# Kernel tuning notes

Hardware: AMD Instinct MI355X
Metric: run time of the kernel (lower is better)

The kernel has to match this reference:

```python
import jax, jax.numpy as jnp
import numpy as np

LN_EPS = 1e-5


def _layer_norm(x, g, b):
    mu = jnp.mean(x, axis=-1, keepdims=True)
    var = jnp.mean(jnp.square(x - mu), axis=-1, keepdims=True)
    return (x - mu) * jax.lax.rsqrt(var + LN_EPS) * g + b


def setup_inputs() -> dict:
    key = jax.random.key(0)
    ks = jax.random.split(key, 8)
    B, S, D = 1, 4096, 1024
    scale = 1.0 / np.sqrt(D)  # keep activations sane (kaiming-ish)
    return {
        "sequences": jax.random.normal(ks[0], (B, S, D), dtype=jnp.float32),
        "W_q": jax.random.normal(ks[1], (D, D), dtype=jnp.float32) * scale,
        "W_k": jax.random.normal(ks[2], (D, D), dtype=jnp.float32) * scale,
        "W_v": jax.random.normal(ks[3], (D, D), dtype=jnp.float32) * scale,
        "W_o": jax.random.normal(ks[4], (D, D), dtype=jnp.float32) * scale,
        "out_w": jax.random.normal(ks[5], (D, D), dtype=jnp.float32) * scale,
        "out_b": jnp.zeros((D,), dtype=jnp.float32),
        "ln_attn_g": jnp.ones((D,), dtype=jnp.float32),
        "ln_attn_b": jnp.zeros((D,), dtype=jnp.float32),
        "ln_lin_g": jnp.ones((D,), dtype=jnp.float32),
        "ln_lin_b": jnp.zeros((D,), dtype=jnp.float32),
    }


def reference(sequences, W_q, W_k, W_v, W_o, out_w, out_b,
              ln_attn_g, ln_attn_b, ln_lin_g, ln_lin_b):
    B, S, D = sequences.shape
    H = 16
    Hd = D // H
    # input_dim == embedding_dim -> no input projection (input_layer is None)
    x = sequences
    q = jnp.einsum('bsd,de->bse', x, W_q)
    k = jnp.einsum('bsd,de->bse', x, W_k)
    v = jnp.einsum('bsd,de->bse', x, W_v)

    def heads(t):  # [B,S,D] -> [B,H,S,Hd]
        return t.reshape(B, S, H, Hd).transpose(0, 2, 1, 3)

    q, k, v = heads(q), heads(k), heads(v)
    scores = jnp.einsum('bhqd,bhkd->bhqk', q, k) / np.sqrt(Hd)  # [B,H,S,S]
    probs = jax.nn.softmax(scores, axis=-1)
    ctx = jnp.einsum('bhqk,bhkd->bhqd', probs, v)
    attn = ctx.transpose(0, 2, 1, 3).reshape(B, S, D)
    mha = _layer_norm(x + jnp.einsum('bsd,de->bse', attn, W_o),
                      ln_attn_g, ln_attn_b)
    lin = jnp.einsum('bsd,ed->bse', mha, out_w) + out_b  # torch Linear: x @ W.T + b
    out = jax.nn.relu(_layer_norm(lin + mha, ln_lin_g, ln_lin_b))
    return out
```

## Files before the change

kernel.cpp:

```cpp
#include <hip/hip_runtime.h>
#include <cstdint>
#include <math.h>

typedef __attribute__((ext_vector_type(8))) short bf16x8;
typedef __attribute__((ext_vector_type(4))) float f32x4;
typedef __attribute__((ext_vector_type(4))) unsigned short u16x4;

__device__ __forceinline__ unsigned short f2bf(float f) {
  union { float f; unsigned int u; } c; c.f = f;
  unsigned int u = c.u;
  return (unsigned short)((u + 0x7FFFu + ((u >> 16) & 1u)) >> 16);
}
__device__ __forceinline__ float bf2f(unsigned short u) {
  return __uint_as_float(((unsigned int)u) << 16);
}

__device__ __forceinline__ unsigned int pack_trunc(float a, float b) {
  return __builtin_amdgcn_perm(__float_as_uint(b), __float_as_uint(a), 0x07060302u);
}

__device__ __forceinline__ float fmax3(float a, float b, float c) {
  return fmaxf(fmaxf(a, b), c);
}

__device__ __forceinline__ void gload_lds16(const void* g, void* l) {
  __builtin_amdgcn_global_load_lds(
      (const __attribute__((address_space(1))) unsigned int*)g,
      (__attribute__((address_space(3))) unsigned int*)l, 16, 0, 0);
}

#define FSYNC(N) do {                                        \
    asm volatile("s_waitcnt vmcnt(" N ")" ::: "memory");     \
    __builtin_amdgcn_s_barrier();                            \
    __builtin_amdgcn_sched_barrier(0);                       \
  } while (0)

__global__ __launch_bounds__(256)
void k_prep(const float* __restrict__ x, unsigned short* __restrict__ xb,
            const float* __restrict__ out_w, unsigned short* __restrict__ OwB,
            const float* __restrict__ w0, const float* __restrict__ w1,
            const float* __restrict__ w2, const float* __restrict__ w3,
            unsigned short* __restrict__ o012, unsigned short* __restrict__ o3) {
  __shared__ float t[32][33];
  const int b = blockIdx.x;
  if (b < 4096) {
    const int m = b >> 10, rem = b & 1023;
    const float* in = m == 0 ? w0 : m == 1 ? w1 : m == 2 ? w2 : w3;
    unsigned short* out = m < 3 ? o012 + (size_t)m * 1048576 : o3;
    const int r0 = (rem >> 5) << 5, c0 = (rem & 31) << 5;
    const int tx = threadIdx.x & 31, ty = threadIdx.x >> 5;
#pragma unroll
    for (int rr = ty; rr < 32; rr += 8) t[rr][tx] = in[(size_t)(r0 + rr) * 1024 + c0 + tx];
    __syncthreads();
#pragma unroll
    for (int cc = ty; cc < 32; cc += 8)
      out[(size_t)(c0 + cc) * 1024 + r0 + tx] = f2bf(t[tx][cc]);
  } else {
    int i = (b - 4096) * 256 + threadIdx.x;
    const float* in;
    unsigned short* out;
    if (i < 1048576) { in = x; out = xb; }
    else { i -= 1048576; if (i >= 262144) return; in = out_w; out = OwB; }
    float4 v = ((const float4*)in)[i];
    u16x4 o;
    o.x = f2bf(v.x); o.y = f2bf(v.y); o.z = f2bf(v.z); o.w = f2bf(v.w);
    ((u16x4*)out)[i] = o;
  }
}

template <int MODE>
__global__ __launch_bounds__(256)
void k_gemm_bt(const unsigned short* __restrict__ A, const unsigned short* __restrict__ BT,
               void* __restrict__ C, unsigned short* __restrict__ VT,
               int M, int N, int K) {
  const int VCOL0 = 2048;
  __shared__ __align__(16) unsigned short As[2][128 * 32];
  __shared__ __align__(16) unsigned short Bs[2][128 * 32];
  const int tid = threadIdx.x;
  const int wid = tid >> 6, lane = tid & 63;
  const int l16 = lane & 15, krow = lane >> 4;
  const int m0 = blockIdx.x * 128, n0 = blockIdx.y * 128;
  const int wr = wid >> 1, wc = wid & 1;

  f32x4 acc[4][4] = {};

  auto stageG = [&](int buf, int k0) {
#pragma unroll
    for (int j = 0; j < 2; j++) {
      int f = j * 256 + tid;
      gload_lds16(A  + (size_t)(m0 + (f >> 2)) * K + k0 + (f & 3) * 8,
                  (char*)As[buf] + (size_t)(j * 256 + wid * 64) * 16);
      gload_lds16(BT + (size_t)(n0 + (f >> 2)) * K + k0 + (f & 3) * 8,
                  (char*)Bs[buf] + (size_t)(j * 256 + wid * 64) * 16);
    }
  };
  auto comp = [&](int buf) {
    bf16x8 a[4], b[4];
#pragma unroll
    for (int i = 0; i < 4; i++) {
      a[i] = *(const bf16x8*)&As[buf][(wr * 64 + i * 16 + l16) * 32 + krow * 8];
      b[i] = *(const bf16x8*)&Bs[buf][(wc * 64 + i * 16 + l16) * 32 + krow * 8];
    }
#pragma unroll
    for (int mi = 0; mi < 4; mi++)
#pragma unroll
      for (int ni = 0; ni < 4; ni++)
        acc[mi][ni] = __builtin_amdgcn_mfma_f32_16x16x32_bf16(a[mi], b[ni], acc[mi][ni], 0, 0, 0);
  };

  stageG(0, 0);
  __syncthreads();
  for (int k0 = 0; k0 < K; k0 += 64) {
    if (k0 + 32 < K) stageG(1, k0 + 32);
    comp(0);
    __syncthreads();
    if (k0 + 64 < K) stageG(0, k0 + 64);
    comp(1);
    __syncthreads();
  }

  if (MODE == 2 && n0 >= VCOL0) {
#pragma unroll
    for (int mi = 0; mi < 4; mi++)
#pragma unroll
      for (int ni = 0; ni < 4; ni++) {
        int col = n0 - VCOL0 + wc * 64 + ni * 16 + l16;
        int row = m0 + wr * 64 + mi * 16 + krow * 4;
        int u0 = row & 63;
        int rowp = (row & ~63) | (u0 & 32) | ((u0 & 12) << 1) | (((u0 >> 4) & 1) << 2);
        uint2 w;
        w.x = (unsigned)f2bf(acc[mi][ni][0]) | ((unsigned)f2bf(acc[mi][ni][1]) << 16);
        w.y = (unsigned)f2bf(acc[mi][ni][2]) | ((unsigned)f2bf(acc[mi][ni][3]) << 16);
        *(uint2*)&VT[(size_t)col * 4096 + rowp] = w;
      }
    return;
  }

#pragma unroll
  for (int mi = 0; mi < 4; mi++)
#pragma unroll
    for (int ni = 0; ni < 4; ni++)
#pragma unroll
      for (int r = 0; r < 4; r++) {
        int row = m0 + wr * 64 + mi * 16 + krow * 4 + r;
        int col = n0 + wc * 64 + ni * 16 + l16;
        float v = acc[mi][ni][r];
        if (MODE) ((unsigned short*)C)[(size_t)row * N + col] = f2bf(v);
        else      ((float*)C)[(size_t)row * N + col] = v;
      }
}

template <int OUTBF>
__global__ __launch_bounds__(256)
void k_gemm_bt_n64(const unsigned short* __restrict__ A, const unsigned short* __restrict__ BT,
                   void* __restrict__ C, int M, int N, int K) {
  __shared__ __align__(16) unsigned short As[2][128 * 32];
  __shared__ __align__(16) unsigned short Bs[2][64 * 32];
  const int tid = threadIdx.x;
  const int wid = tid >> 6, lane = tid & 63;
  const int l16 = lane & 15, krow = lane >> 4;
  const int m0 = blockIdx.x * 128, n0 = blockIdx.y * 64;
  const int wr = wid >> 1, wc = wid & 1;

  f32x4 acc[4][2] = {};

  auto stageG = [&](int buf, int k0) {
#pragma unroll
    for (int j = 0; j < 2; j++) {
      int f = j * 256 + tid;
      gload_lds16(A + (size_t)(m0 + (f >> 2)) * K + k0 + (f & 3) * 8,
                  (char*)As[buf] + (size_t)(j * 256 + wid * 64) * 16);
    }
    gload_lds16(BT + (size_t)(n0 + (tid >> 2)) * K + k0 + (tid & 3) * 8,
                (char*)Bs[buf] + (size_t)(wid * 64) * 16);
  };
  auto comp = [&](int buf) {
    bf16x8 a[4], b[2];
#pragma unroll
    for (int i = 0; i < 4; i++)
      a[i] = *(const bf16x8*)&As[buf][(wr * 64 + i * 16 + l16) * 32 + krow * 8];
#pragma unroll
    for (int i = 0; i < 2; i++)
      b[i] = *(const bf16x8*)&Bs[buf][(wc * 32 + i * 16 + l16) * 32 + krow * 8];
#pragma unroll
    for (int mi = 0; mi < 4; mi++)
#pragma unroll
      for (int ni = 0; ni < 2; ni++)
        acc[mi][ni] = __builtin_amdgcn_mfma_f32_16x16x32_bf16(a[mi], b[ni], acc[mi][ni], 0, 0, 0);
  };

  stageG(0, 0);
  __syncthreads();
  for (int k0 = 0; k0 < K; k0 += 64) {
    if (k0 + 32 < K) stageG(1, k0 + 32);
    comp(0);
    __syncthreads();
    if (k0 + 64 < K) stageG(0, k0 + 64);
    comp(1);
    __syncthreads();
  }

#pragma unroll
  for (int mi = 0; mi < 4; mi++)
#pragma unroll
    for (int ni = 0; ni < 2; ni++)
#pragma unroll
      for (int r = 0; r < 4; r++) {
        int row = m0 + wr * 64 + mi * 16 + krow * 4 + r;
        int col = n0 + wc * 32 + ni * 16 + l16;
        float v = acc[mi][ni][r];
        if (OUTBF) ((unsigned short*)C)[(size_t)row * N + col] = f2bf(v);
        else       ((float*)C)[(size_t)row * N + col] = v;
      }
}

__global__ __launch_bounds__(512)
void k_flash(const unsigned short* __restrict__ QKV, const unsigned short* __restrict__ Vt,
             unsigned short* __restrict__ ctx) {
  __shared__ __align__(16) unsigned short LDS[32768];
  const int tid = threadIdx.x, wid = tid >> 6, lane = tid & 63;
  const int l16 = lane & 15, krow = lane >> 4;
  const int bid = blockIdx.x;
  const int swz = (bid & 7) * 64 + (bid >> 3);
  const int head = swz >> 5, qb = swz & 31;
  const float SC = 0.125f * 1.44269504089f;

  bf16x8 qf[2];
#pragma unroll
  for (int ks = 0; ks < 2; ks++) {
    int row = qb * 128 + wid * 16 + l16;
    qf[ks] = *(const bf16x8*)&QKV[(size_t)row * 3072 + head * 64 + ks * 32 + krow * 8];
  }

  unsigned koff[2][4];
#pragma unroll
  for (int ks = 0; ks < 2; ks++)
#pragma unroll
    for (int ni = 0; ni < 4; ni++) {
      int row = ni * 16 + l16;
      koff[ks][ni] = row * 128 + (((ks * 4 + krow) ^ (row & 7)) << 4);
    }

  const unsigned short* kSrc;
  const unsigned short* vSrc;
  {
    int row = tid >> 3, sch = (tid & 7) ^ (row & 7);
    kSrc = QKV + (size_t)row * 3072 + 1024 + head * 64 + sch * 8;
    vSrc = Vt + (size_t)(head * 64 + row) * 4096 + sch * 8;
  }
  char* dK = (char*)LDS + wid * 1024;
  char* dV = (char*)LDS + 8192 + wid * 1024;

  f32x4 oaccT[4] = {};
  float mrun = -INFINITY;
  float lrun = 0.f;

  auto stage = [&](const int B) {
    gload_lds16(kSrc, dK + B);
    gload_lds16(vSrc, dV + B);
    kSrc += 64 * 3072;
    vSrc += 64;
  };

  auto body = [&](const int B) {
    const char* L = (const char*)LDS;

    f32x4 sacc[4] = {};
    __builtin_amdgcn_s_setprio(1);
#pragma unroll
    for (int ks = 0; ks < 2; ks++)
#pragma unroll
      for (int ni = 0; ni < 4; ni++) {
        bf16x8 kf = *(const bf16x8*)(L + B + koff[ks][ni]);
        sacc[ni] = __builtin_amdgcn_mfma_f32_16x16x32_bf16(kf, qf[ks], sacc[ni], 0, 0, 0);
      }
    __builtin_amdgcn_s_setprio(0);

    float a = fmax3(sacc[0][0], sacc[0][1], sacc[0][2]);
    a = fmax3(a, sacc[0][3], sacc[1][0]);
    a = fmax3(a, sacc[1][1], sacc[1][2]);
    a = fmax3(a, sacc[1][3], sacc[2][0]);
    a = fmax3(a, sacc[2][1], sacc[2][2]);
    a = fmax3(a, sacc[2][3], sacc[3][0]);
    a = fmax3(a, sacc[3][1], sacc[3][2]);
    a = fmaxf(a, sacc[3][3]);

    if (__ballot(__builtin_fmaf(a, SC, -mrun) > 8.f)) {
      a = fmaxf(a, __shfl_xor(a, 16));
      a = fmaxf(a, __shfl_xor(a, 32));
      float mnew = fmaxf(mrun, a * SC);
      float al = __builtin_amdgcn_exp2f(mrun - mnew);
      lrun *= al;
      mrun = mnew;
#pragma unroll
      for (int di = 0; di < 4; di++)
#pragma unroll
        for (int r = 0; r < 4; r++) oaccT[di][r] *= al;
    }

    float ps[4];
#pragma unroll
    for (int ni = 0; ni < 4; ni++) {
      float p0 = __builtin_amdgcn_exp2f(__builtin_fmaf(sacc[ni][0], SC, -mrun));
      float p1 = __builtin_amdgcn_exp2f(__builtin_fmaf(sacc[ni][1], SC, -mrun));
      float p2 = __builtin_amdgcn_exp2f(__builtin_fmaf(sacc[ni][2], SC, -mrun));
      float p3 = __builtin_amdgcn_exp2f(__builtin_fmaf(sacc[ni][3], SC, -mrun));
      sacc[ni][0] = p0; sacc[ni][1] = p1; sacc[ni][2] = p2; sacc[ni][3] = p3;
      ps[ni] = (p0 + p1) + (p2 + p3);
    }
    lrun += (ps[0] + ps[1]) + (ps[2] + ps[3]);

    union PB { unsigned int w[4]; bf16x8 v; };
    PB pb[2];
#pragma unroll
    for (int ks = 0; ks < 2; ks++) {
      pb[ks].w[0] = pack_trunc(sacc[2 * ks][0],     sacc[2 * ks][1]);
      pb[ks].w[1] = pack_trunc(sacc[2 * ks][2],     sacc[2 * ks][3]);
      pb[ks].w[2] = pack_trunc(sacc[2 * ks + 1][0], sacc[2 * ks + 1][1]);
      pb[ks].w[3] = pack_trunc(sacc[2 * ks + 1][2], sacc[2 * ks + 1][3]);
    }

    __builtin_amdgcn_s_setprio(1);
#pragma unroll
    for (int ks = 0; ks < 2; ks++)
#pragma unroll
      for (int di = 0; di < 4; di++) {
        bf16x8 av = *(const bf16x8*)(L + B + 8192 + koff[ks][di]);
        oaccT[di] = __builtin_amdgcn_mfma_f32_16x16x32_bf16(av, pb[ks].v, oaccT[di], 0, 0, 0);
      }
    __builtin_amdgcn_s_setprio(0);
  };

  stage(0);
  stage(16384);
  stage(32768);

  for (int t = 0; t < 60; t += 4) {
    FSYNC("4"); stage(49152); body(0);
    FSYNC("4"); stage(0);     body(16384);
    FSYNC("4"); stage(16384); body(32768);
    FSYNC("4"); stage(32768); body(49152);
  }
  FSYNC("4"); stage(49152); body(0);
  FSYNC("4"); body(16384);
  FSYNC("2"); body(32768);
  FSYNC("0"); body(49152);

  float lr = lrun;
  lr += __shfl_xor(lr, 16);
  lr += __shfl_xor(lr, 32);
  float li = 1.0f / lr;
  int row = qb * 128 + wid * 16 + l16;
#pragma unroll
  for (int di = 0; di < 4; di++) {
    uint2 w;
    w.x = (unsigned)f2bf(oaccT[di][0] * li) | ((unsigned)f2bf(oaccT[di][1] * li) << 16);
    w.y = (unsigned)f2bf(oaccT[di][2] * li) | ((unsigned)f2bf(oaccT[di][3] * li) << 16);
    *(uint2*)&ctx[(size_t)row * 1024 + head * 64 + di * 16 + krow * 4] = w;
  }
}

__global__ __launch_bounds__(256)
void k_ln_res(const float* __restrict__ base, const unsigned short* __restrict__ add,
              const float* __restrict__ g, const float* __restrict__ bb,
              unsigned short* __restrict__ outb) {
  const int r = blockIdx.x, tid = threadIdx.x;
  float4 v = ((const float4*)(base + (size_t)r * 1024))[tid];
  {
    u16x4 w = ((const u16x4*)(add + (size_t)r * 1024))[tid];
    v.x += bf2f(w.x); v.y += bf2f(w.y); v.z += bf2f(w.z); v.w += bf2f(w.w);
  }
  float s1 = v.x + v.y + v.z + v.w;
  float s2 = v.x * v.x + v.y * v.y + v.z * v.z + v.w * v.w;
#pragma unroll
  for (int off = 32; off >= 1; off >>= 1) { s1 += __shfl_xor(s1, off); s2 += __shfl_xor(s2, off); }
  __shared__ float red[8];
  if ((tid & 63) == 0) { red[tid >> 6] = s1; red[4 + (tid >> 6)] = s2; }
  __syncthreads();
  s1 = red[0] + red[1] + red[2] + red[3];
  s2 = red[4] + red[5] + red[6] + red[7];
  const float mu = s1 * (1.0f / 1024.0f);
  const float var = s2 * (1.0f / 1024.0f) - mu * mu;
  const float rs = rsqrtf(var + 1e-5f);
  float4 gv = ((const float4*)g)[tid];
  float4 bv = ((const float4*)bb)[tid];
  u16x4 o;
  o.x = f2bf((v.x - mu) * rs * gv.x + bv.x);
  o.y = f2bf((v.y - mu) * rs * gv.y + bv.y);
  o.z = f2bf((v.z - mu) * rs * gv.z + bv.z);
  o.w = f2bf((v.w - mu) * rs * gv.w + bv.w);
  ((u16x4*)(outb + (size_t)r * 1024))[tid] = o;
}

__global__ __launch_bounds__(256)
void k_ln2(const unsigned short* __restrict__ lin, const unsigned short* __restrict__ mha,
           const float* __restrict__ ob, const float* __restrict__ g,
           const float* __restrict__ bb, float* __restrict__ out) {
  const int r = blockIdx.x, tid = threadIdx.x;
  float4 v;
  {
    u16x4 a = ((const u16x4*)(lin + (size_t)r * 1024))[tid];
    u16x4 w = ((const u16x4*)(mha + (size_t)r * 1024))[tid];
    float4 o = ((const float4*)ob)[tid];
    v.x = bf2f(a.x) + bf2f(w.x) + o.x;
    v.y = bf2f(a.y) + bf2f(w.y) + o.y;
    v.z = bf2f(a.z) + bf2f(w.z) + o.z;
    v.w = bf2f(a.w) + bf2f(w.w) + o.w;
  }
  float s1 = v.x + v.y + v.z + v.w;
  float s2 = v.x * v.x + v.y * v.y + v.z * v.z + v.w * v.w;
#pragma unroll
  for (int off = 32; off >= 1; off >>= 1) { s1 += __shfl_xor(s1, off); s2 += __shfl_xor(s2, off); }
  __shared__ float red[8];
  if ((tid & 63) == 0) { red[tid >> 6] = s1; red[4 + (tid >> 6)] = s2; }
  __syncthreads();
  s1 = red[0] + red[1] + red[2] + red[3];
  s2 = red[4] + red[5] + red[6] + red[7];
  const float mu = s1 * (1.0f / 1024.0f);
  const float var = s2 * (1.0f / 1024.0f) - mu * mu;
  const float rs = rsqrtf(var + 1e-5f);
  float4 gv = ((const float4*)g)[tid];
  float4 bv = ((const float4*)bb)[tid];
  float4 y;
  y.x = fmaxf(0.f, (v.x - mu) * rs * gv.x + bv.x);
  y.y = fmaxf(0.f, (v.y - mu) * rs * gv.y + bv.y);
  y.z = fmaxf(0.f, (v.z - mu) * rs * gv.z + bv.z);
  y.w = fmaxf(0.f, (v.w - mu) * rs * gv.w + bv.w);
  ((float4*)(out + (size_t)r * 1024))[tid] = y;
}

extern "C" void kernel_launch(void* const* d_in, const int* in_sizes, int n_in,
                              void* d_out, int out_size, void* d_ws, size_t ws_size,
                              hipStream_t stream) {
  (void)in_sizes; (void)n_in; (void)out_size; (void)ws_size;
  const float* x     = (const float*)d_in[0];
  const float* Wq    = (const float*)d_in[1];
  const float* Wk    = (const float*)d_in[2];
  const float* Wv    = (const float*)d_in[3];
  const float* Wo    = (const float*)d_in[4];
  const float* out_w = (const float*)d_in[5];
  const float* out_b = (const float*)d_in[6];
  const float* g1    = (const float*)d_in[7];
  const float* b1    = (const float*)d_in[8];
  const float* g2    = (const float*)d_in[9];
  const float* b2    = (const float*)d_in[10];
  float* out = (float*)d_out;

  const size_t MB = 1ull << 20;
  char* ws = (char*)d_ws;
  unsigned short* xb    = (unsigned short*)(ws + 0);
  unsigned short* WqkvT = (unsigned short*)(ws + 8 * MB);
  unsigned short* OwB   = (unsigned short*)(ws + 16 * MB);
  unsigned short* QKV   = (unsigned short*)(ws + 18 * MB);
  unsigned short* Vt    = (unsigned short*)(ws + 42 * MB);
  unsigned short* ctx   = (unsigned short*)(ws + 50 * MB);
  unsigned short* WoT   = (unsigned short*)(ws + 58 * MB);
  unsigned short* proj  = (unsigned short*)(ws + 0);
  unsigned short* mhaB  = (unsigned short*)(ws + 34 * MB);
  unsigned short* lin   = (unsigned short*)(ws + 42 * MB);

  k_prep<<<9216, 256, 0, stream>>>(x, xb, out_w, OwB, Wq, Wk, Wv, Wo, WqkvT, WoT);

  k_gemm_bt<2><<<dim3(32, 24), 256, 0, stream>>>(xb, WqkvT, QKV, Vt, 4096, 3072, 1024);
  k_flash<<<512, 512, 0, stream>>>(QKV, Vt, ctx);
  k_gemm_bt_n64<1><<<dim3(32, 16), 256, 0, stream>>>(ctx, WoT, proj, 4096, 1024, 1024);
  k_ln_res<<<4096, 256, 0, stream>>>(x, proj, g1, b1, mhaB);
  k_gemm_bt_n64<1><<<dim3(32, 16), 256, 0, stream>>>(mhaB, OwB, lin, 4096, 1024, 1024);
  k_ln2<<<4096, 256, 0, stream>>>(lin, mhaB, out_b, g2, b2, out);
}
```

Baseline: 179.7 us.

## Process two query tiles per wave in flash attention with 256-thread blocks

The flash-attention kernel now uses 4 waves per block instead of 8. Each wave handles 32 query rows (two 16-row MFMA tiles), so every K/V fragment read from LDS feeds two MFMAs. To keep the same 64-key tile per stage, each thread issues twice as many global-to-LDS loads, and the vmcnt waits double to match. This halves LDS reads per MFMA and shared per-block overhead, but doubles accumulator and score registers per wave and halves the number of waves available to hide latency.

```diff
diff --git a/kernel.cpp b/kernel.cpp
--- a/kernel.cpp
+++ b/kernel.cpp
@@ -214,7 +214,7 @@
       }
 }
 
-__global__ __launch_bounds__(512)
+__global__ __launch_bounds__(256)
 void k_flash(const unsigned short* __restrict__ QKV, const unsigned short* __restrict__ Vt,
              unsigned short* __restrict__ ctx) {
   __shared__ __align__(16) unsigned short LDS[32768];
@@ -225,12 +225,14 @@
   const int head = swz >> 5, qb = swz & 31;
   const float SC = 0.125f * 1.44269504089f;
 
-  bf16x8 qf[2];
-#pragma unroll
-  for (int ks = 0; ks < 2; ks++) {
-    int row = qb * 128 + wid * 16 + l16;
-    qf[ks] = *(const bf16x8*)&QKV[(size_t)row * 3072 + head * 64 + ks * 32 + krow * 8];
-  }
+  bf16x8 qf[2][2];
+#pragma unroll
+  for (int mi = 0; mi < 2; mi++)
+#pragma unroll
+    for (int ks = 0; ks < 2; ks++) {
+      int row = qb * 128 + wid * 32 + mi * 16 + l16;
+      qf[mi][ks] = *(const bf16x8*)&QKV[(size_t)row * 3072 + head * 64 + ks * 32 + krow * 8];
+    }
 
   unsigned koff[2][4];
 #pragma unroll
@@ -251,13 +253,15 @@
   char* dK = (char*)LDS + wid * 1024;
   char* dV = (char*)LDS + 8192 + wid * 1024;
 
-  f32x4 oaccT[4] = {};
-  float mrun = -INFINITY;
-  float lrun = 0.f;
+  f32x4 oaccT[2][4] = {};
+  float mrun[2] = {-INFINITY, -INFINITY};
+  float lrun[2] = {0.f, 0.f};
 
   auto stage = [&](const int B) {
-    gload_lds16(kSrc, dK + B);
-    gload_lds16(vSrc, dV + B);
+    gload_lds16(kSrc,             dK + B);
+    gload_lds16(kSrc + 32 * 3072, dK + B + 4096);
+    gload_lds16(vSrc,             dV + B);
+    gload_lds16(vSrc + 32 * 4096, dV + B + 4096);
     kSrc += 64 * 3072;
     vSrc += 64;
   };
@@ -265,60 +269,76 @@
   auto body = [&](const int B) {
     const char* L = (const char*)LDS;
 
-    f32x4 sacc[4] = {};
+    f32x4 sacc[2][4] = {};
     __builtin_amdgcn_s_setprio(1);
 #pragma unroll
     for (int ks = 0; ks < 2; ks++)
 #pragma unroll
       for (int ni = 0; ni < 4; ni++) {
         bf16x8 kf = *(const bf16x8*)(L + B + koff[ks][ni]);
-        sacc[ni] = __builtin_amdgcn_mfma_f32_16x16x32_bf16(kf, qf[ks], sacc[ni], 0, 0, 0);
+#pragma unroll
+        for (int mi = 0; mi < 2; mi++)
+          sacc[mi][ni] = __builtin_amdgcn_mfma_f32_16x16x32_bf16(kf, qf[mi][ks], sacc[mi][ni], 0, 0, 0);
       }
     __builtin_amdgcn_s_setprio(0);
 
-    float a = fmax3(sacc[0][0], sacc[0][1], sacc[0][2]);
-    a = fmax3(a, sacc[0][3], sacc[1][0]);
-    a = fmax3(a, sacc[1][1], sacc[1][2]);
-    a = fmax3(a, sacc[1][3], sacc[2][0]);
-    a = fmax3(a, sacc[2][1], sacc[2][2]);
-    a = fmax3(a, sacc[2][3], sacc[3][0]);
-    a = fmax3(a, sacc[3][1], sacc[3][2]);
-    a = fmaxf(a, sacc[3][3]);
-
-    if (__ballot(__builtin_fmaf(a, SC, -mrun) > 8.f)) {
-      a = fmaxf(a, __shfl_xor(a, 16));
-      a = fmaxf(a, __shfl_xor(a, 32));
-      float mnew = fmaxf(mrun, a * SC);
-      float al = __builtin_amdgcn_exp2f(mrun - mnew);
-      lrun *= al;
-      mrun = mnew;
-#pragma unroll
-      for (int di = 0; di < 4; di++)
-#pragma unroll
-        for (int r = 0; r < 4; r++) oaccT[di][r] *= al;
-    }
-
-    float ps[4];
-#pragma unroll
-    for (int ni = 0; ni < 4; ni++) {
-      float p0 = __builtin_amdgcn_exp2f(__builtin_fmaf(sacc[ni][0], SC, -mrun));
-      float p1 = __builtin_amdgcn_exp2f(__builtin_fmaf(sacc[ni][1], SC, -mrun));
-      float p2 = __builtin_amdgcn_exp2f(__builtin_fmaf(sacc[ni][2], SC, -mrun));
-      float p3 = __builtin_amdgcn_exp2f(__builtin_fmaf(sacc[ni][3], SC, -mrun));
-      sacc[ni][0] = p0; sacc[ni][1] = p1; sacc[ni][2] = p2; sacc[ni][3] = p3;
-      ps[ni] = (p0 + p1) + (p2 + p3);
-    }
-    lrun += (ps[0] + ps[1]) + (ps[2] + ps[3]);
+    float pm[2];
+#pragma unroll
+    for (int mi = 0; mi < 2; mi++) {
+      float a = fmax3(sacc[mi][0][0], sacc[mi][0][1], sacc[mi][0][2]);
+      a = fmax3(a, sacc[mi][0][3], sacc[mi][1][0]);
+      a = fmax3(a, sacc[mi][1][1], sacc[mi][1][2]);
+      a = fmax3(a, sacc[mi][1][3], sacc[mi][2][0]);
+      a = fmax3(a, sacc[mi][2][1], sacc[mi][2][2]);
+      a = fmax3(a, sacc[mi][2][3], sacc[mi][3][0]);
+      a = fmax3(a, sacc[mi][3][1], sacc[mi][3][2]);
+      pm[mi] = fmaxf(a, sacc[mi][3][3]);
+    }
+
+    if (__ballot((__builtin_fmaf(pm[0], SC, -mrun[0]) > 8.f) ||
+                 (__builtin_fmaf(pm[1], SC, -mrun[1]) > 8.f))) {
+#pragma unroll
+      for (int mi = 0; mi < 2; mi++) {
+        float a = pm[mi];
+        a = fmaxf(a, __shfl_xor(a, 16));
+        a = fmaxf(a, __shfl_xor(a, 32));
+        float mnew = fmaxf(mrun[mi], a * SC);
+        float al = __builtin_amdgcn_exp2f(mrun[mi] - mnew);
+        lrun[mi] *= al;
+        mrun[mi] = mnew;
+#pragma unroll
+        for (int di = 0; di < 4; di++)
+#pragma unroll
+          for (int r = 0; r < 4; r++) oaccT[mi][di][r] *= al;
+      }
+    }
+
+#pragma unroll
+    for (int mi = 0; mi < 2; mi++) {
+      float ps[4];
+#pragma unroll
+      for (int ni = 0; ni < 4; ni++) {
+        float p0 = __builtin_amdgcn_exp2f(__builtin_fmaf(sacc[mi][ni][0], SC, -mrun[mi]));
+        float p1 = __builtin_amdgcn_exp2f(__builtin_fmaf(sacc[mi][ni][1], SC, -mrun[mi]));
+        float p2 = __builtin_amdgcn_exp2f(__builtin_fmaf(sacc[mi][ni][2], SC, -mrun[mi]));
+        float p3 = __builtin_amdgcn_exp2f(__builtin_fmaf(sacc[mi][ni][3], SC, -mrun[mi]));
+        sacc[mi][ni][0] = p0; sacc[mi][ni][1] = p1; sacc[mi][ni][2] = p2; sacc[mi][ni][3] = p3;
+        ps[ni] = (p0 + p1) + (p2 + p3);
+      }
+      lrun[mi] += (ps[0] + ps[1]) + (ps[2] + ps[3]);
+    }
 
     union PB { unsigned int w[4]; bf16x8 v; };
-    PB pb[2];
-#pragma unroll
-    for (int ks = 0; ks < 2; ks++) {
-      pb[ks].w[0] = pack_trunc(sacc[2 * ks][0],     sacc[2 * ks][1]);
-      pb[ks].w[1] = pack_trunc(sacc[2 * ks][2],     sacc[2 * ks][3]);
-      pb[ks].w[2] = pack_trunc(sacc[2 * ks + 1][0], sacc[2 * ks + 1][1]);
-      pb[ks].w[3] = pack_trunc(sacc[2 * ks + 1][2], sacc[2 * ks + 1][3]);
-    }
+    PB pb[2][2];
+#pragma unroll
+    for (int mi = 0; mi < 2; mi++)
+#pragma unroll
+      for (int ks = 0; ks < 2; ks++) {
+        pb[mi][ks].w[0] = pack_trunc(sacc[mi][2 * ks][0],     sacc[mi][2 * ks][1]);
+        pb[mi][ks].w[1] = pack_trunc(sacc[mi][2 * ks][2],     sacc[mi][2 * ks][3]);
+        pb[mi][ks].w[2] = pack_trunc(sacc[mi][2 * ks + 1][0], sacc[mi][2 * ks + 1][1]);
+        pb[mi][ks].w[3] = pack_trunc(sacc[mi][2 * ks + 1][2], sacc[mi][2 * ks + 1][3]);
+      }
 
     __builtin_amdgcn_s_setprio(1);
 #pragma unroll
@@ -326,7 +346,9 @@
 #pragma unroll
       for (int di = 0; di < 4; di++) {
         bf16x8 av = *(const bf16x8*)(L + B + 8192 + koff[ks][di]);
-        oaccT[di] = __builtin_amdgcn_mfma_f32_16x16x32_bf16(av, pb[ks].v, oaccT[di], 0, 0, 0);
+#pragma unroll
+        for (int mi = 0; mi < 2; mi++)
+          oaccT[mi][di] = __builtin_amdgcn_mfma_f32_16x16x32_bf16(av, pb[mi][ks].v, oaccT[mi][di], 0, 0, 0);
       }
     __builtin_amdgcn_s_setprio(0);
   };
@@ -336,27 +358,30 @@
   stage(32768);
 
   for (int t = 0; t < 60; t += 4) {
-    FSYNC("4"); stage(49152); body(0);
-    FSYNC("4"); stage(0);     body(16384);
-    FSYNC("4"); stage(16384); body(32768);
-    FSYNC("4"); stage(32768); body(49152);
-  }
-  FSYNC("4"); stage(49152); body(0);
-  FSYNC("4"); body(16384);
-  FSYNC("2"); body(32768);
+    FSYNC("8"); stage(49152); body(0);
+    FSYNC("8"); stage(0);     body(16384);
+    FSYNC("8"); stage(16384); body(32768);
+    FSYNC("8"); stage(32768); body(49152);
+  }
+  FSYNC("8"); stage(49152); body(0);
+  FSYNC("8"); body(16384);
+  FSYNC("4"); body(32768);
   FSYNC("0"); body(49152);
 
-  float lr = lrun;
-  lr += __shfl_xor(lr, 16);
-  lr += __shfl_xor(lr, 32);
-  float li = 1.0f / lr;
-  int row = qb * 128 + wid * 16 + l16;
-#pragma unroll
-  for (int di = 0; di < 4; di++) {
-    uint2 w;
-    w.x = (unsigned)f2bf(oaccT[di][0] * li) | ((unsigned)f2bf(oaccT[di][1] * li) << 16);
-    w.y = (unsigned)f2bf(oaccT[di][2] * li) | ((unsigned)f2bf(oaccT[di][3] * li) << 16);
-    *(uint2*)&ctx[(size_t)row * 1024 + head * 64 + di * 16 + krow * 4] = w;
+#pragma unroll
+  for (int mi = 0; mi < 2; mi++) {
+    float lr = lrun[mi];
+    lr += __shfl_xor(lr, 16);
+    lr += __shfl_xor(lr, 32);
+    float li = 1.0f / lr;
+    int row = qb * 128 + wid * 32 + mi * 16 + l16;
+#pragma unroll
+    for (int di = 0; di < 4; di++) {
+      uint2 w;
+      w.x = (unsigned)f2bf(oaccT[mi][di][0] * li) | ((unsigned)f2bf(oaccT[mi][di][1] * li) << 16);
+      w.y = (unsigned)f2bf(oaccT[mi][di][2] * li) | ((unsigned)f2bf(oaccT[mi][di][3] * li) << 16);
+      *(uint2*)&ctx[(size_t)row * 1024 + head * 64 + di * 16 + krow * 4] = w;
+    }
   }
 }
 
@@ -462,7 +487,7 @@
   k_prep<<<9216, 256, 0, stream>>>(x, xb, out_w, OwB, Wq, Wk, Wv, Wo, WqkvT, WoT);
 
   k_gemm_bt<2><<<dim3(32, 24), 256, 0, stream>>>(xb, WqkvT, QKV, Vt, 4096, 3072, 1024);
-  k_flash<<<512, 512, 0, stream>>>(QKV, Vt, ctx);
+  k_flash<<<512, 256, 0, stream>>>(QKV, Vt, ctx);
   k_gemm_bt_n64<1><<<dim3(32, 16), 256, 0, stream>>>(ctx, WoT, proj, 4096, 1024, 1024);
   k_ln_res<<<4096, 256, 0, stream>>>(x, proj, g1, b1, mhaB);
   k_gemm_bt_n64<1><<<dim3(32, 16), 256, 0, stream>>>(mhaB, OwB, lin, 4096, 1024, 1024);
```

Result: no change. 182.8 us (+1.7%).
